# Kernel optimization log

Hardware: AMD Instinct MI355X
Metric: run time of the kernel (lower is better)

## Reference

```python
import jax, jax.numpy as jnp
import numpy as np

D_MODEL = 1024
N_HEAD = 16
SEQ = 4096
BATCH = 1


def setup_inputs() -> dict:
    key = jax.random.key(0)
    k1, k2, k3 = jax.random.split(key, 3)
    scale_in = 1.0 / np.sqrt(D_MODEL)
    x = jax.random.normal(k1, (BATCH, SEQ, D_MODEL), dtype=jnp.float32)
    # torch nn.Linear(d, 3d, bias=False): y = x @ W.T with W [3d, d].
    # We store the transposed matrix [d, 3d] so y = x @ w_qkv (same math).
    w_qkv = jax.random.normal(k2, (D_MODEL, 3 * D_MODEL), dtype=jnp.float32) * scale_in
    w_proj = jax.random.normal(k3, (D_MODEL, D_MODEL), dtype=jnp.float32) * scale_in
    return {"x": x, "w_qkv": w_qkv, "w_proj": w_proj}


def _attention(x, w_qkv, w_proj):
    bsz, t, c = x.shape
    d_head = c // N_HEAD
    qkv = x @ w_qkv                              # [b, t, 3c]
    q, k, v = jnp.split(qkv, 3, axis=-1)

    def reshape(tensor):
        # [b, t, c] -> [b, h, t, d]
        return tensor.reshape(bsz, t, N_HEAD, d_head).transpose(0, 2, 1, 3)

    q, k, v = reshape(q), reshape(k), reshape(v)
    scale = 1.0 / jnp.sqrt(jnp.asarray(d_head, dtype=q.dtype))
    scores = jnp.einsum("bhqd,bhkd->bhqk", q, k) * scale  # [b, h, t, t]
    causal = jnp.tril(jnp.ones((t, t), dtype=bool))
    scores = jnp.where(causal, scores, jnp.asarray(-jnp.inf, dtype=scores.dtype))
    attn = jax.nn.softmax(scores, axis=-1)
    y = jnp.einsum("bhqk,bhkd->bhqd", attn, v)            # [b, h, t, d]
    y = y.transpose(0, 2, 1, 3).reshape(bsz, t, c)        # [b, t, c]
    return y @ w_proj


def reference(x, w_qkv, w_proj):
    return _attention(x, w_qkv, w_proj)
```

## Files before the change

kernel.cpp:

```cpp
#include <hip/hip_runtime.h>
#include <hip/hip_bf16.h>


typedef unsigned short ushort_t;
typedef __attribute__((ext_vector_type(8))) __bf16 bf16x8;
typedef __attribute__((ext_vector_type(8))) unsigned short ushort8;
typedef __attribute__((ext_vector_type(4))) unsigned short ushort4v;
typedef __attribute__((ext_vector_type(4))) float f32x4;

#define SWZ(row, e) (((row) << 6) + ((e) ^ (((row) & 7) << 3)))

__device__ inline unsigned short f2bf(float f) {
  union { float f; unsigned int u; } v;
  v.f = f;
  unsigned int r = v.u + 0x7fffu + ((v.u >> 16) & 1u);
  return (unsigned short)(r >> 16);
}

__device__ __forceinline__ float fast_exp2(float x) {
  float r;
  asm("v_exp_f32 %0, %1" : "=v"(r) : "v"(x));
  return r;
}

__device__ __forceinline__ void gl_lds16(const void* g, void* l) {
  __builtin_amdgcn_global_load_lds((const __attribute__((address_space(1))) void*)g,
                                   (__attribute__((address_space(3))) void*)l, 16, 0, 0);
}

__global__ __launch_bounds__(256) void cvt_f32_bf16(const float* __restrict__ in,
                                                    ushort_t* __restrict__ out) {
  const size_t i = ((size_t)blockIdx.x * 256 + threadIdx.x) * 4;
  const float4 v = *(const float4*)(in + i);
  ushort4v o;
  o.x = f2bf(v.x); o.y = f2bf(v.y); o.z = f2bf(v.z); o.w = f2bf(v.w);
  *(ushort4v*)(out + i) = o;
}

__global__ __launch_bounds__(256) void transpose_f32_bf16(const float* __restrict__ in,
                                                          ushort_t* __restrict__ out,
                                                          int R, int C) {
  __shared__ ushort_t tile[32][33];
  const int r0 = blockIdx.y * 32, c0 = blockIdx.x * 32;
  const int tx = threadIdx.x, ty = threadIdx.y;
  #pragma unroll
  for (int j = 0; j < 32; j += 8)
    tile[ty + j][tx] = f2bf(in[(size_t)(r0 + ty + j) * C + c0 + tx]);
  __syncthreads();
  #pragma unroll
  for (int j = 0; j < 32; j += 8)
    out[(size_t)(c0 + ty + j) * R + r0 + tx] = tile[tx][ty + j];
}

__global__ __launch_bounds__(256) void transpose_bf16_ld(const ushort_t* __restrict__ in,
                                                         ushort_t* __restrict__ out,
                                                         int in_ld, int out_ld) {
  __shared__ ushort_t tile[32][33];
  const int r0 = blockIdx.y * 32, c0 = blockIdx.x * 32;
  const int tx = threadIdx.x, ty = threadIdx.y;
  #pragma unroll
  for (int j = 0; j < 32; j += 8)
    tile[ty + j][tx] = in[(size_t)(r0 + ty + j) * in_ld + c0 + tx];
  __syncthreads();
  #pragma unroll
  for (int j = 0; j < 32; j += 8)
    out[(size_t)(c0 + ty + j) * out_ld + r0 + tx] = tile[tx][ty + j];
}

__global__ __launch_bounds__(256) void gemm_bt_bf16out(const ushort_t* __restrict__ A,
                                                       const ushort_t* __restrict__ Bt,
                                                       ushort_t* __restrict__ C,
                                                       int M, int N, int K) {
  __shared__ __attribute__((aligned(16))) ushort_t As[128 * 64];
  __shared__ __attribute__((aligned(16))) ushort_t Bs[128 * 64];
  const int tid = threadIdx.x;
  const int lane = tid & 63;
  const int wave = tid >> 6;
  const int wy = wave >> 1, wx = wave & 1;
  const int quad = lane >> 4, l16 = lane & 15;
  const size_t bm = (size_t)blockIdx.y * 128;
  const size_t bn = (size_t)blockIdx.x * 128;

  const f32x4 fzero = {0.f, 0.f, 0.f, 0.f};
  f32x4 acc[4][4];
  #pragma unroll
  for (int i = 0; i < 4; ++i)
    #pragma unroll
    for (int j = 0; j < 4; ++j) acc[i][j] = fzero;

  for (int k0 = 0; k0 < K; k0 += 64) {
    #pragma unroll
    for (int i = 0; i < 4; ++i) {
      int c = (wave * 4 + i) * 64 + lane;
      int row = c >> 3, col = (c & 7) * 8;
      gl_lds16(A + (bm + row) * K + k0 + col, As + c * 8);
      gl_lds16(Bt + (bn + row) * K + k0 + col, Bs + c * 8);
    }
    __syncthreads();
    #pragma unroll
    for (int ks = 0; ks < 2; ++ks) {
      bf16x8 af[4], bb[4];
      #pragma unroll
      for (int mt = 0; mt < 4; ++mt)
        af[mt] = *(const bf16x8*)(As + (wy * 64 + mt * 16 + l16) * 64 + ks * 32 + quad * 8);
      #pragma unroll
      for (int nt = 0; nt < 4; ++nt)
        bb[nt] = *(const bf16x8*)(Bs + (wx * 64 + nt * 16 + l16) * 64 + ks * 32 + quad * 8);
      #pragma unroll
      for (int mt = 0; mt < 4; ++mt)
        #pragma unroll
        for (int nt = 0; nt < 4; ++nt)
          acc[mt][nt] = __builtin_amdgcn_mfma_f32_16x16x32_bf16(af[mt], bb[nt], acc[mt][nt], 0, 0, 0);
    }
    __syncthreads();
  }
  const float sc = (blockIdx.x < 8) ? 0.18033688f : 1.0f;
  #pragma unroll
  for (int mt = 0; mt < 4; ++mt)
    #pragma unroll
    for (int nt = 0; nt < 4; ++nt)
      #pragma unroll
      for (int r = 0; r < 4; ++r)
        C[(bm + wy * 64 + mt * 16 + quad * 4 + r) * N + bn + wx * 64 + nt * 16 + l16] =
            f2bf(acc[mt][nt][r] * sc);
}

__global__ __launch_bounds__(256) void gemm_bt_f32out(const ushort_t* __restrict__ A,
                                                      const ushort_t* __restrict__ Bt,
                                                      float* __restrict__ C,
                                                      int M, int N, int K, int lda) {
  __shared__ __attribute__((aligned(16))) ushort_t As[128 * 64];
  __shared__ __attribute__((aligned(16))) ushort_t Bs[128 * 64];
  const int tid = threadIdx.x;
  const int lane = tid & 63;
  const int wave = tid >> 6;
  const int wy = wave >> 1, wx = wave & 1;
  const int quad = lane >> 4, l16 = lane & 15;
  const size_t bm = (size_t)blockIdx.y * 128;
  const size_t bn = (size_t)blockIdx.x * 128;

  const f32x4 fzero = {0.f, 0.f, 0.f, 0.f};
  f32x4 acc[4][4];
  #pragma unroll
  for (int i = 0; i < 4; ++i)
    #pragma unroll
    for (int j = 0; j < 4; ++j) acc[i][j] = fzero;

  for (int k0 = 0; k0 < K; k0 += 64) {
    #pragma unroll
    for (int i = 0; i < 4; ++i) {
      int c = (wave * 4 + i) * 64 + lane;
      int row = c >> 3, col = (c & 7) * 8;
      gl_lds16(A + (bm + row) * lda + k0 + col, As + c * 8);
      gl_lds16(Bt + (bn + row) * K + k0 + col, Bs + c * 8);
    }
    __syncthreads();
    #pragma unroll
    for (int ks = 0; ks < 2; ++ks) {
      bf16x8 af[4], bb[4];
      #pragma unroll
      for (int mt = 0; mt < 4; ++mt)
        af[mt] = *(const bf16x8*)(As + (wy * 64 + mt * 16 + l16) * 64 + ks * 32 + quad * 8);
      #pragma unroll
      for (int nt = 0; nt < 4; ++nt)
        bb[nt] = *(const bf16x8*)(Bs + (wx * 64 + nt * 16 + l16) * 64 + ks * 32 + quad * 8);
      #pragma unroll
      for (int mt = 0; mt < 4; ++mt)
        #pragma unroll
        for (int nt = 0; nt < 4; ++nt)
          acc[mt][nt] = __builtin_amdgcn_mfma_f32_16x16x32_bf16(af[mt], bb[nt], acc[mt][nt], 0, 0, 0);
    }
    __syncthreads();
  }
  #pragma unroll
  for (int mt = 0; mt < 4; ++mt)
    #pragma unroll
    for (int nt = 0; nt < 4; ++nt)
      #pragma unroll
      for (int r = 0; r < 4; ++r)
        C[(bm + wy * 64 + mt * 16 + quad * 4 + r) * N + bn + wx * 64 + nt * 16 + l16] =
            acc[mt][nt][r];
}

__device__ __forceinline__ void strip_exp_store(ushort_t* Ps, const f32x4* s, int kb,
                                                int sbase, int srowPs, int quad, int l16) {
  const bool masked = (kb + 63 > sbase);
  #pragma unroll
  for (int nt = 0; nt < 4; ++nt) {
    float p[4];
    #pragma unroll
    for (int r = 0; r < 4; ++r) {
      float xv = s[nt][r];
      if (masked) {
        int kkg = kb + nt * 16 + quad * 4 + r;
        xv = (kkg <= sbase + l16) ? xv : -30000.f;
      }
      p[r] = fast_exp2(xv);
    }
    unsigned int u01, u23;
    asm("v_cvt_pk_bf16_f32 %0, %1, %2" : "=v"(u01) : "v"(p[0]), "v"(p[1]));
    asm("v_cvt_pk_bf16_f32 %0, %1, %2" : "=v"(u23) : "v"(p[2]), "v"(p[3]));
    uint2 pu; pu.x = u01; pu.y = u23;
    *(uint2*)(Ps + SWZ(srowPs, nt * 16 + quad * 4)) = pu;
  }
}

__global__ __launch_bounds__(256, 4) void attn_fwd(const ushort_t* __restrict__ qkv,
                                                   const ushort_t* __restrict__ vT,
                                                   ushort_t* __restrict__ y) {
  __shared__ __attribute__((aligned(16))) ushort_t Ks[2][64 * 64];
  __shared__ __attribute__((aligned(16))) ushort_t Vt[2][64 * 64];
  __shared__ __attribute__((aligned(16))) ushort_t Ps[64 * 64];
  const int head = blockIdx.x;
  const int by = blockIdx.y;
  const int g = by >> 4, r4 = by & 15;
  const int qt = (g == 0) ? r4 : (g == 1) ? (63 - r4) : (g == 2) ? (16 + r4) : (47 - r4);
  const int qb = qt * 64;
  const int ntiles = qt + 1;
  const int tid = threadIdx.x;
  const int lane = tid & 63, wave = tid >> 6;
  const int quad = lane >> 4, l16 = lane & 15;
  const int hoff = head * 64;
  const int wrow = wave * 16;
  const int srow = tid >> 2, scol = (tid & 3) * 16;

  bf16x8 bq[2];
  #pragma unroll
  for (int ks = 0; ks < 2; ++ks)
    bq[ks] = *(const bf16x8*)(qkv + (size_t)(qb + wrow + l16) * 3072 + hoff +
                              ks * 32 + quad * 8);

  bf16x8 ones;
  #pragma unroll
  for (int i = 0; i < 8; ++i) ones[i] = (__bf16)1.0f;

  ushort8 kreg[2], vreg[2];
  #pragma unroll
  for (int i = 0; i < 2; ++i) {
    kreg[i] = *(const ushort8*)(qkv + (size_t)srow * 3072 + 1024 + hoff + scol + i * 8);
    vreg[i] = *(const ushort8*)(vT + (size_t)(hoff + srow) * 4096 + scol + i * 8);
  }
  #pragma unroll
  for (int i = 0; i < 2; ++i) {
    *(ushort8*)(Ks[0] + SWZ(srow, scol + i * 8)) = kreg[i];
    *(ushort8*)(Vt[0] + SWZ(srow, scol + i * 8)) = vreg[i];
  }
  #pragma unroll
  for (int i = 0; i < 2; ++i) {
    kreg[i] = *(const ushort8*)(qkv + (size_t)(64 + srow) * 3072 + 1024 + hoff + scol + i * 8);
    vreg[i] = *(const ushort8*)(vT + (size_t)(hoff + srow) * 4096 + 64 + scol + i * 8);
  }

  const f32x4 fzero = {0.f, 0.f, 0.f, 0.f};
  f32x4 o0[4], ol0 = fzero;
  #pragma unroll
  for (int nt = 0; nt < 4; ++nt) o0[nt] = fzero;

  for (int t = 0; t < ntiles; ++t) {
    const int cur = t & 1;
    __syncthreads();

    f32x4 s0[4];
    #pragma unroll
    for (int nt = 0; nt < 4; ++nt) s0[nt] = fzero;
    __builtin_amdgcn_s_setprio(1);
    #pragma unroll
    for (int ks = 0; ks < 2; ++ks)
      #pragma unroll
      for (int nt = 0; nt < 4; ++nt) {
        bf16x8 ak = *(const bf16x8*)(Ks[cur] + SWZ(nt * 16 + l16, ks * 32 + quad * 8));
        s0[nt] = __builtin_amdgcn_mfma_f32_16x16x32_bf16(ak, bq[ks], s0[nt], 0, 0, 0);
      }
    __builtin_amdgcn_s_setprio(0);

    if (t + 1 < ntiles) {
      #pragma unroll
      for (int i = 0; i < 2; ++i) {
        *(ushort8*)(Ks[1 - cur] + SWZ(srow, scol + i * 8)) = kreg[i];
        *(ushort8*)(Vt[1 - cur] + SWZ(srow, scol + i * 8)) = vreg[i];
      }
      if (t + 2 < ntiles) {
        const int kb2 = (t + 2) * 64;
        #pragma unroll
        for (int i = 0; i < 2; ++i) {
          kreg[i] = *(const ushort8*)(qkv + (size_t)(kb2 + srow) * 3072 + 1024 + hoff +
                                      scol + i * 8);
          vreg[i] = *(const ushort8*)(vT + (size_t)(hoff + srow) * 4096 + kb2 + scol + i * 8);
        }
      }
    }

    const int kb = t * 64;
    strip_exp_store(Ps, s0, kb, qb + wrow, wrow + l16, quad, l16);

    __builtin_amdgcn_s_setprio(1);
    #pragma unroll
    for (int ks = 0; ks < 2; ++ks) {
      bf16x8 bp0 = *(const bf16x8*)(Ps + SWZ(wrow + l16, ks * 32 + quad * 8));
      #pragma unroll
      for (int nt = 0; nt < 4; ++nt) {
        bf16x8 av = *(const bf16x8*)(Vt[cur] + SWZ(nt * 16 + l16, ks * 32 + quad * 8));
        o0[nt] = __builtin_amdgcn_mfma_f32_16x16x32_bf16(av, bp0, o0[nt], 0, 0, 0);
      }
      ol0 = __builtin_amdgcn_mfma_f32_16x16x32_bf16(ones, bp0, ol0, 0, 0, 0);
    }
    __builtin_amdgcn_s_setprio(0);
  }

  const float inv0 = 1.0f / ol0[0];
  #pragma unroll
  for (int nt = 0; nt < 4; ++nt) {
    ushort4v ov0;
    #pragma unroll
    for (int r = 0; r < 4; ++r) ov0[r] = f2bf(o0[nt][r] * inv0);
    *(ushort4v*)(y + (size_t)(qb + wrow + l16) * 3072 + hoff + nt * 16 + quad * 4) = ov0;
  }
}

extern "C" void kernel_launch(void* const* d_in, const int* in_sizes, int n_in,
                              void* d_out, int out_size, void* d_ws, size_t ws_size,
                              hipStream_t stream) {
  const float* x = (const float*)d_in[0];
  const float* w_qkv = (const float*)d_in[1];
  const float* w_proj = (const float*)d_in[2];
  float* out = (float*)d_out;

  ushort_t* ws = (ushort_t*)d_ws;
  ushort_t* qkv = ws;
  ushort_t* wqkvT = ws + (size_t)4096 * 3072;
  ushort_t* vT = wqkvT;
  ushort_t* yb = qkv + 2048;
  ushort_t* wprojT = wqkvT;
  ushort_t* xb = (ushort_t*)d_out;

  cvt_f32_bf16<<<4096, 256, 0, stream>>>(x, xb);
  transpose_f32_bf16<<<dim3(96, 32), dim3(32, 8), 0, stream>>>(w_qkv, wqkvT, 1024, 3072);
  gemm_bt_bf16out<<<dim3(24, 32), 256, 0, stream>>>(xb, wqkvT, qkv, 4096, 3072, 1024);
  transpose_bf16_ld<<<dim3(32, 128), dim3(32, 8), 0, stream>>>(qkv + 2048, vT, 3072, 4096);
  attn_fwd<<<dim3(16, 64), 256, 0, stream>>>(qkv, vT, yb);
  transpose_f32_bf16<<<dim3(32, 32), dim3(32, 8), 0, stream>>>(w_proj, wprojT, 1024, 1024);
  gemm_bt_f32out<<<dim3(8, 32), 256, 0, stream>>>(yb, wprojT, out, 4096, 1024, 1024, 3072);
}
```

Baseline: 226.7 us.

## Fuse V transpose into QKV GEMM epilogue and shrink projection GEMM tile

The QKV GEMM blocks that produce V now transpose their tile through shared memory and write V^T directly, removing the separate transpose kernel and its extra global round trip. V^T is placed in the unused second half of the output buffer so it no longer aliases the weight buffer still being read. The output projection GEMM uses 128x64 tiles instead of 128x128, doubling the block count for better CU occupancy at the cost of less reuse per block.

```diff
diff --git a/kernel.cpp b/kernel.cpp
--- a/kernel.cpp
+++ b/kernel.cpp
@@ -6,6 +6,7 @@
 typedef __attribute__((ext_vector_type(8))) __bf16 bf16x8;
 typedef __attribute__((ext_vector_type(8))) unsigned short ushort8;
 typedef __attribute__((ext_vector_type(4))) unsigned short ushort4v;
+typedef __attribute__((ext_vector_type(2))) unsigned short ushort2v;
 typedef __attribute__((ext_vector_type(4))) float f32x4;
 
 #define SWZ(row, e) (((row) << 6) + ((e) ^ (((row) & 7) << 3)))
@@ -52,27 +53,14 @@
     out[(size_t)(c0 + ty + j) * R + r0 + tx] = tile[tx][ty + j];
 }
 
-__global__ __launch_bounds__(256) void transpose_bf16_ld(const ushort_t* __restrict__ in,
-                                                         ushort_t* __restrict__ out,
-                                                         int in_ld, int out_ld) {
-  __shared__ ushort_t tile[32][33];
-  const int r0 = blockIdx.y * 32, c0 = blockIdx.x * 32;
-  const int tx = threadIdx.x, ty = threadIdx.y;
-  #pragma unroll
-  for (int j = 0; j < 32; j += 8)
-    tile[ty + j][tx] = in[(size_t)(r0 + ty + j) * in_ld + c0 + tx];
-  __syncthreads();
-  #pragma unroll
-  for (int j = 0; j < 32; j += 8)
-    out[(size_t)(c0 + ty + j) * out_ld + r0 + tx] = tile[tx][ty + j];
-}
-
 __global__ __launch_bounds__(256) void gemm_bt_bf16out(const ushort_t* __restrict__ A,
                                                        const ushort_t* __restrict__ Bt,
                                                        ushort_t* __restrict__ C,
+                                                       ushort_t* __restrict__ vT,
                                                        int M, int N, int K) {
-  __shared__ __attribute__((aligned(16))) ushort_t As[128 * 64];
-  __shared__ __attribute__((aligned(16))) ushort_t Bs[128 * 64];
+  __shared__ __attribute__((aligned(16))) ushort_t smem[128 * 64 * 2];
+  ushort_t* As = smem;
+  ushort_t* Bs = smem + 128 * 64;
   const int tid = threadIdx.x;
   const int lane = tid & 63;
   const int wave = tid >> 6;
@@ -114,15 +102,46 @@
     }
     __syncthreads();
   }
-  const float sc = (blockIdx.x < 8) ? 0.18033688f : 1.0f;
-  #pragma unroll
-  for (int mt = 0; mt < 4; ++mt)
-    #pragma unroll
-    for (int nt = 0; nt < 4; ++nt)
-      #pragma unroll
-      for (int r = 0; r < 4; ++r)
-        C[(bm + wy * 64 + mt * 16 + quad * 4 + r) * N + bn + wx * 64 + nt * 16 + l16] =
-            f2bf(acc[mt][nt][r] * sc);
+
+  if (blockIdx.x < 16) {
+    const float sc = (blockIdx.x < 8) ? 0.18033688f : 1.0f;
+    #pragma unroll
+    for (int mt = 0; mt < 4; ++mt)
+      #pragma unroll
+      for (int nt = 0; nt < 4; ++nt)
+        #pragma unroll
+        for (int r = 0; r < 4; ++r)
+          C[(bm + wy * 64 + mt * 16 + quad * 4 + r) * N + bn + wx * 64 + nt * 16 + l16] =
+              f2bf(acc[mt][nt][r] * sc);
+  } else {
+    const int vbase = (int)bn - 2048;
+    #pragma unroll
+    for (int p = 0; p < 2; ++p) {
+      if (wx == p) {
+        #pragma unroll
+        for (int nt = 0; nt < 4; ++nt)
+          #pragma unroll
+          for (int mt = 0; mt < 4; ++mt)
+            #pragma unroll
+            for (int i = 0; i < 2; ++i) {
+              ushort2v pr;
+              pr.x = f2bf(acc[mt][nt][2 * i]);
+              pr.y = f2bf(acc[mt][nt][2 * i + 1]);
+              *(ushort2v*)(smem + (nt * 16 + l16) * 136 + wy * 64 + mt * 16 + quad * 4 +
+                           2 * i) = pr;
+            }
+      }
+      __syncthreads();
+      #pragma unroll
+      for (int j = 0; j < 4; ++j) {
+        int v = (tid >> 4) + j * 16;
+        int row0 = (tid & 15) * 8;
+        ushort8 val = *(const ushort8*)(smem + v * 136 + row0);
+        *(ushort8*)(vT + (size_t)(vbase + p * 64 + v) * 4096 + bm + row0) = val;
+      }
+      __syncthreads();
+    }
+  }
 }
 
 __global__ __launch_bounds__(256) void gemm_bt_f32out(const ushort_t* __restrict__ A,
@@ -130,21 +149,21 @@
                                                       float* __restrict__ C,
                                                       int M, int N, int K, int lda) {
   __shared__ __attribute__((aligned(16))) ushort_t As[128 * 64];
-  __shared__ __attribute__((aligned(16))) ushort_t Bs[128 * 64];
+  __shared__ __attribute__((aligned(16))) ushort_t Bs[64 * 64];
   const int tid = threadIdx.x;
   const int lane = tid & 63;
   const int wave = tid >> 6;
   const int wy = wave >> 1, wx = wave & 1;
   const int quad = lane >> 4, l16 = lane & 15;
   const size_t bm = (size_t)blockIdx.y * 128;
-  const size_t bn = (size_t)blockIdx.x * 128;
+  const size_t bn = (size_t)blockIdx.x * 64;
 
   const f32x4 fzero = {0.f, 0.f, 0.f, 0.f};
-  f32x4 acc[4][4];
+  f32x4 acc[4][2];
   #pragma unroll
   for (int i = 0; i < 4; ++i)
     #pragma unroll
-    for (int j = 0; j < 4; ++j) acc[i][j] = fzero;
+    for (int j = 0; j < 2; ++j) acc[i][j] = fzero;
 
   for (int k0 = 0; k0 < K; k0 += 64) {
     #pragma unroll
@@ -152,22 +171,27 @@
       int c = (wave * 4 + i) * 64 + lane;
       int row = c >> 3, col = (c & 7) * 8;
       gl_lds16(A + (bm + row) * lda + k0 + col, As + c * 8);
+    }
+    #pragma unroll
+    for (int i = 0; i < 2; ++i) {
+      int c = (wave * 2 + i) * 64 + lane;
+      int row = c >> 3, col = (c & 7) * 8;
       gl_lds16(Bt + (bn + row) * K + k0 + col, Bs + c * 8);
     }
     __syncthreads();
     #pragma unroll
     for (int ks = 0; ks < 2; ++ks) {
-      bf16x8 af[4], bb[4];
+      bf16x8 af[4], bb[2];
       #pragma unroll
       for (int mt = 0; mt < 4; ++mt)
         af[mt] = *(const bf16x8*)(As + (wy * 64 + mt * 16 + l16) * 64 + ks * 32 + quad * 8);
       #pragma unroll
-      for (int nt = 0; nt < 4; ++nt)
-        bb[nt] = *(const bf16x8*)(Bs + (wx * 64 + nt * 16 + l16) * 64 + ks * 32 + quad * 8);
+      for (int nt = 0; nt < 2; ++nt)
+        bb[nt] = *(const bf16x8*)(Bs + (wx * 32 + nt * 16 + l16) * 64 + ks * 32 + quad * 8);
       #pragma unroll
       for (int mt = 0; mt < 4; ++mt)
         #pragma unroll
-        for (int nt = 0; nt < 4; ++nt)
+        for (int nt = 0; nt < 2; ++nt)
           acc[mt][nt] = __builtin_amdgcn_mfma_f32_16x16x32_bf16(af[mt], bb[nt], acc[mt][nt], 0, 0, 0);
     }
     __syncthreads();
@@ -175,10 +199,10 @@
   #pragma unroll
   for (int mt = 0; mt < 4; ++mt)
     #pragma unroll
-    for (int nt = 0; nt < 4; ++nt)
+    for (int nt = 0; nt < 2; ++nt)
       #pragma unroll
       for (int r = 0; r < 4; ++r)
-        C[(bm + wy * 64 + mt * 16 + quad * 4 + r) * N + bn + wx * 64 + nt * 16 + l16] =
+        C[(bm + wy * 64 + mt * 16 + quad * 4 + r) * N + bn + wx * 32 + nt * 16 + l16] =
             acc[mt][nt][r];
 }
 
@@ -328,16 +352,15 @@
   ushort_t* ws = (ushort_t*)d_ws;
   ushort_t* qkv = ws;
   ushort_t* wqkvT = ws + (size_t)4096 * 3072;
-  ushort_t* vT = wqkvT;
   ushort_t* yb = qkv + 2048;
   ushort_t* wprojT = wqkvT;
   ushort_t* xb = (ushort_t*)d_out;
+  ushort_t* vT = (ushort_t*)d_out + (size_t)4096 * 1024;
 
   cvt_f32_bf16<<<4096, 256, 0, stream>>>(x, xb);
   transpose_f32_bf16<<<dim3(96, 32), dim3(32, 8), 0, stream>>>(w_qkv, wqkvT, 1024, 3072);
-  gemm_bt_bf16out<<<dim3(24, 32), 256, 0, stream>>>(xb, wqkvT, qkv, 4096, 3072, 1024);
-  transpose_bf16_ld<<<dim3(32, 128), dim3(32, 8), 0, stream>>>(qkv + 2048, vT, 3072, 4096);
+  gemm_bt_bf16out<<<dim3(24, 32), 256, 0, stream>>>(xb, wqkvT, qkv, vT, 4096, 3072, 1024);
   attn_fwd<<<dim3(16, 64), 256, 0, stream>>>(qkv, vT, yb);
   transpose_f32_bf16<<<dim3(32, 32), dim3(32, 8), 0, stream>>>(w_proj, wprojT, 1024, 1024);
-  gemm_bt_f32out<<<dim3(8, 32), 256, 0, stream>>>(yb, wprojT, out, 4096, 1024, 1024, 3072);
-}
+  gemm_bt_f32out<<<dim3(16, 32), 256, 0, stream>>>(yb, wprojT, out, 4096, 1024, 1024, 3072);
+}
```

Measured after the change: 216.3 us. 4.6% less time.
